# Kernel tuning notes

Hardware: AMD Instinct MI355X
Metric: run time of the kernel (lower is better)

Reference implementation:

```python
import jax, jax.numpy as jnp
import numpy as np

NUM_CHANNELS = 256
NUM_HEADS = 8
HEAD_DIM = NUM_CHANNELS // NUM_HEADS


def setup_inputs() -> dict:
    key = jax.random.key(0)
    k1, k2, k3, k4, k5 = jax.random.split(key, 5)
    C = NUM_CHANNELS
    s = 1.0 / np.sqrt(C)
    image = jax.random.normal(k1, (8, C, 32, 32), dtype=jnp.float32)
    # kqv_projection: Linear(C, 3C); mix_heads: Linear(C, C). Stored as [in, out].
    w_kqv = jax.random.uniform(k2, (C, 3 * C), minval=-s, maxval=s, dtype=jnp.float32)
    b_kqv = jax.random.uniform(k3, (3 * C,), minval=-s, maxval=s, dtype=jnp.float32)
    w_mix = jax.random.uniform(k4, (C, C), minval=-s, maxval=s, dtype=jnp.float32)
    b_mix = jax.random.uniform(k5, (C,), minval=-s, maxval=s, dtype=jnp.float32)
    return {"image": image, "w_kqv": w_kqv, "b_kqv": b_kqv, "w_mix": w_mix, "b_mix": b_mix}


def _masked_attention(seq, w_kqv, b_kqv, w_mix, b_mix):
    # seq: [N, T, C]
    N, T, C = seq.shape
    H, D = NUM_HEADS, HEAD_DIM
    projected = seq @ w_kqv + b_kqv            # [N, T, 3C]
    k, q, v = jnp.split(projected, 3, axis=-1)  # order: keys, queries, values
    # split heads -> [N, H, T, D]
    k = k.reshape(N, T, H, D).transpose(0, 2, 1, 3)
    q = q.reshape(N, T, H, D).transpose(0, 2, 1, 3)
    v = v.reshape(N, T, H, D).transpose(0, 2, 1, 3)
    logits = jnp.einsum('nhtd,nhsd->nhts', q, k) / jnp.sqrt(jnp.float32(D))
    causal = jnp.tril(jnp.ones((T, T), dtype=bool))
    logits = jnp.where(causal, logits, -jnp.inf)
    weights = jax.nn.softmax(logits, axis=-1)
    out = jnp.einsum('nhts,nhsd->nhtd', weights, v)  # [N, H, T, D]
    out = out.transpose(0, 2, 1, 3).reshape(N, T, C)  # combine heads
    return out @ w_mix + b_mix


def reference(image, w_kqv, b_kqv, w_mix, b_mix):
    N, C, Hh, Ww = image.shape
    seq = image.transpose(0, 2, 3, 1).reshape(N, Hh * Ww, C)
    attn = _masked_attention(seq, w_kqv, b_kqv, w_mix, b_mix)
    attn = attn.reshape(N, Hh, Ww, C).transpose(0, 3, 1, 2)
    return attn + image
```

## Files before the change

### kernel.cpp

```cpp
#include <hip/hip_runtime.h>
#include <math.h>

constexpr int NB  = 8;
constexpr int C   = 256;
constexpr int T   = 1024;
constexpr int NH  = 8;
constexpr int HD  = 32;
constexpr int C3  = 768;

constexpr float QSCALE = 0.25503489422229562f;

typedef __attribute__((ext_vector_type(8))) short bf16x8;
typedef __attribute__((ext_vector_type(4))) float f32x4;

__device__ inline short f2bf(float f) {
    unsigned u = __float_as_uint(f);
    u += 0x7FFF + ((u >> 16) & 1);
    return (short)(u >> 16);
}
__device__ inline short f2bf_trunc(float f) {
    return (short)(__float_as_uint(f) >> 16);
}

__global__ __launch_bounds__(256) void xpose_bf16(const float* __restrict__ image,
                                                  const float* __restrict__ wkqv,
                                                  const float* __restrict__ wmix,
                                                  short* __restrict__ seqb,
                                                  short* __restrict__ wkqvT,
                                                  short* __restrict__ wmixT) {
    __shared__ float Ld[32][33];
    const int bid = blockIdx.x;
    const float* src; short* dst; int srcStride;
    if (bid < 2048) {
        int nb = bid >> 8, rem = bid & 255, cb = rem >> 5, tb = rem & 31;
        src = image + ((size_t)nb * C + cb * 32) * T + tb * 32;
        dst = seqb + ((size_t)nb * T + tb * 32) * C + cb * 32;
        srcStride = T;
    } else if (bid < 2240) {
        int id = bid - 2048, jb = id >> 3, cb = id & 7;
        src = wkqv + (size_t)(cb * 32) * C3 + jb * 32;
        dst = wkqvT + (size_t)(jb * 32) * C + cb * 32;
        srcStride = C3;
    } else {
        int id = bid - 2240, jb = id >> 3, cb = id & 7;
        src = wmix + (size_t)(cb * 32) * C + jb * 32;
        dst = wmixT + (size_t)(jb * 32) * C + cb * 32;
        srcStride = C;
    }
    const int r = threadIdx.x >> 3, c4 = (threadIdx.x & 7) * 4;
    float4 v = *(const float4*)&src[(size_t)r * srcStride + c4];
    Ld[r][c4 + 0] = v.x; Ld[r][c4 + 1] = v.y; Ld[r][c4 + 2] = v.z; Ld[r][c4 + 3] = v.w;
    __syncthreads();
    short4 o = { f2bf(Ld[c4 + 0][r]), f2bf(Ld[c4 + 1][r]),
                 f2bf(Ld[c4 + 2][r]), f2bf(Ld[c4 + 3][r]) };
    *(short4*)&dst[(size_t)r * C + c4] = o;
}

__global__ __launch_bounds__(256) void kqv_mfma(const short* __restrict__ seqb,
                                                const short* __restrict__ wkqvT,
                                                const float* __restrict__ bkqv,
                                                short* __restrict__ Kb,
                                                short* __restrict__ Qb,
                                                short* __restrict__ Vb) {
    __shared__ __align__(16) short As[64][40];
    __shared__ __align__(16) short Bs[64][40];
    const int tid = threadIdx.x;
    const int n0 = blockIdx.x * 64;
    const int m0 = blockIdx.y * 64;
    const int nb = m0 >> 10, t0 = m0 & 1023;
    const int wv = tid >> 6, lane = tid & 63;
    const int m = lane & 15, quad = lane >> 4;
    const int sr = tid >> 2, sc8 = (tid & 3) * 8;

    f32x4 acc[4];
    const f32x4 z = {0.f, 0.f, 0.f, 0.f};
    #pragma unroll
    for (int j = 0; j < 4; ++j) acc[j] = z;

    bf16x8 areg = *(const bf16x8*)&seqb[(size_t)(m0 + sr) * C + sc8];
    bf16x8 breg = *(const bf16x8*)&wkqvT[(size_t)(n0 + sr) * C + sc8];

    for (int k0 = 0; k0 < C; k0 += 32) {
        __syncthreads();
        *(bf16x8*)&As[sr][sc8] = areg;
        *(bf16x8*)&Bs[sr][sc8] = breg;
        if (k0 + 32 < C) {
            areg = *(const bf16x8*)&seqb[(size_t)(m0 + sr) * C + k0 + 32 + sc8];
            breg = *(const bf16x8*)&wkqvT[(size_t)(n0 + sr) * C + k0 + 32 + sc8];
        }
        __syncthreads();
        bf16x8 a = *(const bf16x8*)&As[16 * wv + m][8 * quad];
        bf16x8 b[4];
        #pragma unroll
        for (int j = 0; j < 4; ++j) b[j] = *(const bf16x8*)&Bs[16 * j + m][8 * quad];
        #pragma unroll
        for (int j = 0; j < 4; ++j)
            acc[j] = __builtin_amdgcn_mfma_f32_16x16x32_bf16(a, b[j], acc[j], 0, 0, 0);
    }

    #pragma unroll
    for (int j = 0; j < 4; ++j) {
        int jj = n0 + 16 * j + m;
        int chunk = jj >> 8, hh = (jj >> 5) & 7, d = jj & 31;
        short* dst = (chunk == 0) ? Kb : (chunk == 1) ? Qb : Vb;
        float bias = bkqv[jj];
        float mul = (chunk == 1) ? QSCALE : 1.0f;
        size_t base = (size_t)(nb * NH + hh) * T * HD + d;
        int t = t0 + 16 * wv + 4 * quad;
        #pragma unroll
        for (int r = 0; r < 4; ++r)
            dst[base + (size_t)(t + r) * HD] = f2bf((acc[j][r] + bias) * mul);
    }
}

__global__ __launch_bounds__(256) void attn_mfma(const short* __restrict__ Kb,
                                                 const short* __restrict__ Qb,
                                                 const short* __restrict__ Vb,
                                                 short* __restrict__ attnb) {
    const int qb = 7 - blockIdx.x;
    const int h  = blockIdx.y;
    const int nb = blockIdx.z;
    const int tid  = threadIdx.x;
    const int wv   = tid >> 6;
    const int lane = tid & 63;
    const int m    = lane & 15;
    const int quad = lane >> 4;

    __shared__ __align__(16) short Qs[128][40];
    __shared__ __align__(16) short Ks[2][64][40];
    __shared__ __align__(16) short Vt[2][32][72];
    __shared__ __align__(16) short Ps[128][72];

    const int q0  = qb * 128;
    const int nst = 2 * qb + 2;
    const size_t hb = (size_t)(nb * NH + h) * T * HD;
    const short* Kp = Kb + hb;
    const short* Qp = Qb + hb;
    const short* Vp = Vb + hb;
    const int sr = tid >> 2, sc8 = (tid & 3) * 8;
    const f32x4 z = {0.f, 0.f, 0.f, 0.f};

    bf16x8 qr0  = *(const bf16x8*)&Qp[(size_t)(q0 + sr) * HD + sc8];
    bf16x8 qr1  = *(const bf16x8*)&Qp[(size_t)(q0 + 64 + sr) * HD + sc8];
    bf16x8 kreg = *(const bf16x8*)&Kp[(size_t)sr * HD + sc8];
    bf16x8 vreg = *(const bf16x8*)&Vp[(size_t)sr * HD + sc8];
    *(bf16x8*)&Qs[sr][sc8]      = qr0;
    *(bf16x8*)&Qs[64 + sr][sc8] = qr1;
    *(bf16x8*)&Ks[0][sr][sc8]   = kreg;
    #pragma unroll
    for (int i2 = 0; i2 < 8; ++i2) Vt[0][sc8 + i2][sr] = vreg[i2];

    f32x4 O[2][2] = {{z, z}, {z, z}};
    float lp[2][4] = {};

    for (int st = 0; st < nst; ++st) {
        const int p = st & 1;
        __syncthreads();
        if (st + 1 < nst) {
            kreg = *(const bf16x8*)&Kp[(size_t)((st + 1) * 64 + sr) * HD + sc8];
            vreg = *(const bf16x8*)&Vp[(size_t)((st + 1) * 64 + sr) * HD + sc8];
        }

        bf16x8 bk[4];
        #pragma unroll
        for (int j = 0; j < 4; ++j) bk[j] = *(const bf16x8*)&Ks[p][16 * j + m][8 * quad];
        f32x4 S[2][4];
        #pragma unroll
        for (int i = 0; i < 2; ++i) {
            bf16x8 aq = *(const bf16x8*)&Qs[32 * wv + 16 * i + m][8 * quad];
            #pragma unroll
            for (int j = 0; j < 4; ++j)
                S[i][j] = __builtin_amdgcn_mfma_f32_16x16x32_bf16(aq, bk[j], z, 0, 0, 0);
        }

        const bool msk = (st >= 2 * qb);
        const int s0 = st * 64;
        #pragma unroll
        for (int i = 0; i < 2; ++i) {
            const int qr_base = q0 + 32 * wv + 16 * i + 4 * quad;
            #pragma unroll
            for (int j = 0; j < 4; ++j) {
                const int sc = s0 + 16 * j + m;
                #pragma unroll
                for (int r = 0; r < 4; ++r) {
                    float e = __builtin_amdgcn_exp2f(S[i][j][r]);
                    if (msk && sc > qr_base + r) e = 0.f;
                    lp[i][r] += e;
                    Ps[32 * wv + 16 * i + 4 * quad + r][16 * j + m] = f2bf_trunc(e);
                }
            }
        }

        #pragma unroll
        for (int kc = 0; kc < 2; ++kc) {
            bf16x8 ap0 = *(const bf16x8*)&Ps[32 * wv + m][32 * kc + 8 * quad];
            bf16x8 ap1 = *(const bf16x8*)&Ps[32 * wv + 16 + m][32 * kc + 8 * quad];
            bf16x8 b0  = *(const bf16x8*)&Vt[p][m][32 * kc + 8 * quad];
            bf16x8 b1  = *(const bf16x8*)&Vt[p][16 + m][32 * kc + 8 * quad];
            O[0][0] = __builtin_amdgcn_mfma_f32_16x16x32_bf16(ap0, b0, O[0][0], 0, 0, 0);
            O[0][1] = __builtin_amdgcn_mfma_f32_16x16x32_bf16(ap0, b1, O[0][1], 0, 0, 0);
            O[1][0] = __builtin_amdgcn_mfma_f32_16x16x32_bf16(ap1, b0, O[1][0], 0, 0, 0);
            O[1][1] = __builtin_amdgcn_mfma_f32_16x16x32_bf16(ap1, b1, O[1][1], 0, 0, 0);
        }

        if (st + 1 < nst) {
            const int pn = p ^ 1;
            *(bf16x8*)&Ks[pn][sr][sc8] = kreg;
            #pragma unroll
            for (int i2 = 0; i2 < 8; ++i2) Vt[pn][sc8 + i2][sr] = vreg[i2];
        }
    }

    #pragma unroll
    for (int i = 0; i < 2; ++i)
        #pragma unroll
        for (int r = 0; r < 4; ++r) {
            float l = lp[i][r];
            l += __shfl_xor(l, 1);
            l += __shfl_xor(l, 2);
            l += __shfl_xor(l, 4);
            l += __shfl_xor(l, 8);
            float inv = 1.f / l;
            int row = q0 + 32 * wv + 16 * i + 4 * quad + r;
            short* op = attnb + ((size_t)(nb * T + row)) * C + h * HD;
            op[m]      = f2bf(O[i][0][r] * inv);
            op[16 + m] = f2bf(O[i][1][r] * inv);
        }
}

__global__ __launch_bounds__(256) void mix_mfma(const short* __restrict__ attnb,
                                                const short* __restrict__ wmixT,
                                                const float* __restrict__ bmix,
                                                const float* __restrict__ image,
                                                float* __restrict__ out) {
    __shared__ __align__(16) short As[64][40];
    __shared__ __align__(16) short Bs[64][40];
    const int tid = threadIdx.x;
    const int n0 = blockIdx.x * 64;
    const int m0 = blockIdx.y * 64;
    const int nb = m0 >> 10, t0 = m0 & 1023;
    const int wv = tid >> 6, lane = tid & 63;
    const int m = lane & 15, quad = lane >> 4;
    const int sr = tid >> 2, sc8 = (tid & 3) * 8;

    f32x4 acc[4];
    const f32x4 z = {0.f, 0.f, 0.f, 0.f};
    #pragma unroll
    for (int j = 0; j < 4; ++j) acc[j] = z;

    bf16x8 areg = *(const bf16x8*)&attnb[(size_t)(m0 + sr) * C + sc8];
    bf16x8 breg = *(const bf16x8*)&wmixT[(size_t)(n0 + sr) * C + sc8];

    for (int k0 = 0; k0 < C; k0 += 32) {
        __syncthreads();
        *(bf16x8*)&As[sr][sc8] = areg;
        *(bf16x8*)&Bs[sr][sc8] = breg;
        if (k0 + 32 < C) {
            areg = *(const bf16x8*)&attnb[(size_t)(m0 + sr) * C + k0 + 32 + sc8];
            breg = *(const bf16x8*)&wmixT[(size_t)(n0 + sr) * C + k0 + 32 + sc8];
        }
        __syncthreads();
        bf16x8 a = *(const bf16x8*)&As[16 * wv + m][8 * quad];
        bf16x8 b[4];
        #pragma unroll
        for (int j = 0; j < 4; ++j) b[j] = *(const bf16x8*)&Bs[16 * j + m][8 * quad];
        #pragma unroll
        for (int j = 0; j < 4; ++j)
            acc[j] = __builtin_amdgcn_mfma_f32_16x16x32_bf16(a, b[j], acc[j], 0, 0, 0);
    }

    const int tb = t0 + 16 * wv + 4 * quad;
    #pragma unroll
    for (int j = 0; j < 4; ++j) {
        int c = n0 + 16 * j + m;
        float bias = bmix[c];
        size_t o = (size_t)(nb * C + c) * T + tb;
        float4 img = *(const float4*)&image[o];
        float4 res = { acc[j][0] + bias + img.x,
                       acc[j][1] + bias + img.y,
                       acc[j][2] + bias + img.z,
                       acc[j][3] + bias + img.w };
        *(float4*)&out[o] = res;
    }
}

extern "C" void kernel_launch(void* const* d_in, const int* in_sizes, int n_in,
                              void* d_out, int out_size, void* d_ws, size_t ws_size,
                              hipStream_t stream) {
    const float* image = (const float*)d_in[0];
    const float* w_kqv = (const float*)d_in[1];
    const float* b_kqv = (const float*)d_in[2];
    const float* w_mix = (const float*)d_in[3];
    const float* b_mix = (const float*)d_in[4];
    float* out = (float*)d_out;

    short* seqb  = (short*)d_ws;
    short* wkqvT = seqb  + (size_t)NB * T * C;
    short* wmixT = wkqvT + (size_t)C3 * C;
    short* Kb    = wmixT + (size_t)C * C;
    short* Qb    = Kb    + (size_t)NB * NH * T * HD;
    short* Vb    = Qb    + (size_t)NB * NH * T * HD;
    short* attnb = Vb    + (size_t)NB * NH * T * HD;

    xpose_bf16<<<2304, 256, 0, stream>>>(image, w_kqv, w_mix, seqb, wkqvT, wmixT);
    kqv_mfma<<<dim3(C3 / 64, NB * T / 64), 256, 0, stream>>>(seqb, wkqvT, b_kqv, Kb, Qb, Vb);
    attn_mfma<<<dim3(8, NH, NB), 256, 0, stream>>>(Kb, Qb, Vb, attnb);
    mix_mfma<<<dim3(C / 64, NB * T / 64), 256, 0, stream>>>(attnb, wmixT, b_mix, image, out);
}
```

Baseline: 115.8 us.

## Fuse image transpose into KQV GEMM and pair causal query blocks in attention

The KQV projection now reads the fp32 NCHW image directly, converting to bf16 and transposing while staging its A tile into shared memory. This drops the separate image transpose pass and the seqb round-trip through global memory. The attention kernel now launches half as many blocks, and each block handles a short and a long causal query block (qb and 7-qb) so every block does the same amount of work. The cost is coalesced-but-strided fp32 loads in the GEMM and fewer, longer attention blocks, which lowers the available parallelism.

```diff
diff --git a/kernel.cpp b/kernel.cpp
--- a/kernel.cpp
+++ b/kernel.cpp
@@ -22,27 +22,20 @@
     return (short)(__float_as_uint(f) >> 16);
 }
 
-__global__ __launch_bounds__(256) void xpose_bf16(const float* __restrict__ image,
-                                                  const float* __restrict__ wkqv,
-                                                  const float* __restrict__ wmix,
-                                                  short* __restrict__ seqb,
-                                                  short* __restrict__ wkqvT,
-                                                  short* __restrict__ wmixT) {
+__global__ __launch_bounds__(256) void xpose_w(const float* __restrict__ wkqv,
+                                               const float* __restrict__ wmix,
+                                               short* __restrict__ wkqvT,
+                                               short* __restrict__ wmixT) {
     __shared__ float Ld[32][33];
     const int bid = blockIdx.x;
     const float* src; short* dst; int srcStride;
-    if (bid < 2048) {
-        int nb = bid >> 8, rem = bid & 255, cb = rem >> 5, tb = rem & 31;
-        src = image + ((size_t)nb * C + cb * 32) * T + tb * 32;
-        dst = seqb + ((size_t)nb * T + tb * 32) * C + cb * 32;
-        srcStride = T;
-    } else if (bid < 2240) {
-        int id = bid - 2048, jb = id >> 3, cb = id & 7;
+    if (bid < 192) {
+        int jb = bid >> 3, cb = bid & 7;
         src = wkqv + (size_t)(cb * 32) * C3 + jb * 32;
         dst = wkqvT + (size_t)(jb * 32) * C + cb * 32;
         srcStride = C3;
     } else {
-        int id = bid - 2240, jb = id >> 3, cb = id & 7;
+        int id = bid - 192, jb = id >> 3, cb = id & 7;
         src = wmix + (size_t)(cb * 32) * C + jb * 32;
         dst = wmixT + (size_t)(jb * 32) * C + cb * 32;
         srcStride = C;
@@ -56,7 +49,7 @@
     *(short4*)&dst[(size_t)r * C + c4] = o;
 }
 
-__global__ __launch_bounds__(256) void kqv_mfma(const short* __restrict__ seqb,
+__global__ __launch_bounds__(256) void kqv_mfma(const float* __restrict__ image,
                                                 const short* __restrict__ wkqvT,
                                                 const float* __restrict__ bkqv,
                                                 short* __restrict__ Kb,
@@ -71,21 +64,32 @@
     const int wv = tid >> 6, lane = tid & 63;
     const int m = lane & 15, quad = lane >> 4;
     const int sr = tid >> 2, sc8 = (tid & 3) * 8;
+    const int am = tid & 63, ak8 = (tid >> 6) * 8;
+
+    const float* imgn = image + (size_t)nb * C * T;
 
     f32x4 acc[4];
     const f32x4 z = {0.f, 0.f, 0.f, 0.f};
     #pragma unroll
     for (int j = 0; j < 4; ++j) acc[j] = z;
 
-    bf16x8 areg = *(const bf16x8*)&seqb[(size_t)(m0 + sr) * C + sc8];
+    float fa[8];
+    #pragma unroll
+    for (int i = 0; i < 8; ++i)
+        fa[i] = imgn[(size_t)(ak8 + i) * T + t0 + am];
     bf16x8 breg = *(const bf16x8*)&wkqvT[(size_t)(n0 + sr) * C + sc8];
 
     for (int k0 = 0; k0 < C; k0 += 32) {
         __syncthreads();
-        *(bf16x8*)&As[sr][sc8] = areg;
+        short4 alo = { f2bf(fa[0]), f2bf(fa[1]), f2bf(fa[2]), f2bf(fa[3]) };
+        short4 ahi = { f2bf(fa[4]), f2bf(fa[5]), f2bf(fa[6]), f2bf(fa[7]) };
+        *(short4*)&As[am][ak8]     = alo;
+        *(short4*)&As[am][ak8 + 4] = ahi;
         *(bf16x8*)&Bs[sr][sc8] = breg;
         if (k0 + 32 < C) {
-            areg = *(const bf16x8*)&seqb[(size_t)(m0 + sr) * C + k0 + 32 + sc8];
+            #pragma unroll
+            for (int i = 0; i < 8; ++i)
+                fa[i] = imgn[(size_t)(k0 + 32 + ak8 + i) * T + t0 + am];
             breg = *(const bf16x8*)&wkqvT[(size_t)(n0 + sr) * C + k0 + 32 + sc8];
         }
         __syncthreads();
@@ -117,7 +121,7 @@
                                                  const short* __restrict__ Qb,
                                                  const short* __restrict__ Vb,
                                                  short* __restrict__ attnb) {
-    const int qb = 7 - blockIdx.x;
+    const int qp = blockIdx.x;
     const int h  = blockIdx.y;
     const int nb = blockIdx.z;
     const int tid  = threadIdx.x;
@@ -131,8 +135,6 @@
     __shared__ __align__(16) short Vt[2][32][72];
     __shared__ __align__(16) short Ps[128][72];
 
-    const int q0  = qb * 128;
-    const int nst = 2 * qb + 2;
     const size_t hb = (size_t)(nb * NH + h) * T * HD;
     const short* Kp = Kb + hb;
     const short* Qp = Qb + hb;
@@ -140,92 +142,99 @@
     const int sr = tid >> 2, sc8 = (tid & 3) * 8;
     const f32x4 z = {0.f, 0.f, 0.f, 0.f};
 
-    bf16x8 qr0  = *(const bf16x8*)&Qp[(size_t)(q0 + sr) * HD + sc8];
-    bf16x8 qr1  = *(const bf16x8*)&Qp[(size_t)(q0 + 64 + sr) * HD + sc8];
-    bf16x8 kreg = *(const bf16x8*)&Kp[(size_t)sr * HD + sc8];
-    bf16x8 vreg = *(const bf16x8*)&Vp[(size_t)sr * HD + sc8];
-    *(bf16x8*)&Qs[sr][sc8]      = qr0;
-    *(bf16x8*)&Qs[64 + sr][sc8] = qr1;
-    *(bf16x8*)&Ks[0][sr][sc8]   = kreg;
-    #pragma unroll
-    for (int i2 = 0; i2 < 8; ++i2) Vt[0][sc8 + i2][sr] = vreg[i2];
-
-    f32x4 O[2][2] = {{z, z}, {z, z}};
-    float lp[2][4] = {};
-
-    for (int st = 0; st < nst; ++st) {
-        const int p = st & 1;
-        __syncthreads();
-        if (st + 1 < nst) {
-            kreg = *(const bf16x8*)&Kp[(size_t)((st + 1) * 64 + sr) * HD + sc8];
-            vreg = *(const bf16x8*)&Vp[(size_t)((st + 1) * 64 + sr) * HD + sc8];
+    #pragma unroll 1
+    for (int pp = 0; pp < 2; ++pp) {
+        const int qb  = pp ? 7 - qp : qp;
+        const int q0  = qb * 128;
+        const int nst = 2 * qb + 2;
+
+        __syncthreads();
+
+        *(bf16x8*)&Qs[sr][sc8]      = *(const bf16x8*)&Qp[(size_t)(q0 + sr) * HD + sc8];
+        *(bf16x8*)&Qs[64 + sr][sc8] = *(const bf16x8*)&Qp[(size_t)(q0 + 64 + sr) * HD + sc8];
+        bf16x8 kreg = *(const bf16x8*)&Kp[(size_t)sr * HD + sc8];
+        bf16x8 vreg = *(const bf16x8*)&Vp[(size_t)sr * HD + sc8];
+        *(bf16x8*)&Ks[0][sr][sc8] = kreg;
+        #pragma unroll
+        for (int i2 = 0; i2 < 8; ++i2) Vt[0][sc8 + i2][sr] = vreg[i2];
+
+        f32x4 O[2][2] = {{z, z}, {z, z}};
+        float lp[2][4] = {};
+
+        for (int st = 0; st < nst; ++st) {
+            const int p = st & 1;
+            __syncthreads();
+            if (st + 1 < nst) {
+                kreg = *(const bf16x8*)&Kp[(size_t)((st + 1) * 64 + sr) * HD + sc8];
+                vreg = *(const bf16x8*)&Vp[(size_t)((st + 1) * 64 + sr) * HD + sc8];
+            }
+
+            bf16x8 bk[4];
+            #pragma unroll
+            for (int j = 0; j < 4; ++j) bk[j] = *(const bf16x8*)&Ks[p][16 * j + m][8 * quad];
+            f32x4 S[2][4];
+            #pragma unroll
+            for (int i = 0; i < 2; ++i) {
+                bf16x8 aq = *(const bf16x8*)&Qs[32 * wv + 16 * i + m][8 * quad];
+                #pragma unroll
+                for (int j = 0; j < 4; ++j)
+                    S[i][j] = __builtin_amdgcn_mfma_f32_16x16x32_bf16(aq, bk[j], z, 0, 0, 0);
+            }
+
+            const bool msk = (st >= 2 * qb);
+            const int s0 = st * 64;
+            #pragma unroll
+            for (int i = 0; i < 2; ++i) {
+                const int qr_base = q0 + 32 * wv + 16 * i + 4 * quad;
+                #pragma unroll
+                for (int j = 0; j < 4; ++j) {
+                    const int sc = s0 + 16 * j + m;
+                    #pragma unroll
+                    for (int r = 0; r < 4; ++r) {
+                        float e = __builtin_amdgcn_exp2f(S[i][j][r]);
+                        if (msk && sc > qr_base + r) e = 0.f;
+                        lp[i][r] += e;
+                        Ps[32 * wv + 16 * i + 4 * quad + r][16 * j + m] = f2bf_trunc(e);
+                    }
+                }
+            }
+
+            #pragma unroll
+            for (int kc = 0; kc < 2; ++kc) {
+                bf16x8 ap0 = *(const bf16x8*)&Ps[32 * wv + m][32 * kc + 8 * quad];
+                bf16x8 ap1 = *(const bf16x8*)&Ps[32 * wv + 16 + m][32 * kc + 8 * quad];
+                bf16x8 b0  = *(const bf16x8*)&Vt[p][m][32 * kc + 8 * quad];
+                bf16x8 b1  = *(const bf16x8*)&Vt[p][16 + m][32 * kc + 8 * quad];
+                O[0][0] = __builtin_amdgcn_mfma_f32_16x16x32_bf16(ap0, b0, O[0][0], 0, 0, 0);
+                O[0][1] = __builtin_amdgcn_mfma_f32_16x16x32_bf16(ap0, b1, O[0][1], 0, 0, 0);
+                O[1][0] = __builtin_amdgcn_mfma_f32_16x16x32_bf16(ap1, b0, O[1][0], 0, 0, 0);
+                O[1][1] = __builtin_amdgcn_mfma_f32_16x16x32_bf16(ap1, b1, O[1][1], 0, 0, 0);
+            }
+
+            if (st + 1 < nst) {
+                const int pn = p ^ 1;
+                *(bf16x8*)&Ks[pn][sr][sc8] = kreg;
+                #pragma unroll
+                for (int i2 = 0; i2 < 8; ++i2) Vt[pn][sc8 + i2][sr] = vreg[i2];
+            }
         }
 
-        bf16x8 bk[4];
-        #pragma unroll
-        for (int j = 0; j < 4; ++j) bk[j] = *(const bf16x8*)&Ks[p][16 * j + m][8 * quad];
-        f32x4 S[2][4];
-        #pragma unroll
-        for (int i = 0; i < 2; ++i) {
-            bf16x8 aq = *(const bf16x8*)&Qs[32 * wv + 16 * i + m][8 * quad];
-            #pragma unroll
-            for (int j = 0; j < 4; ++j)
-                S[i][j] = __builtin_amdgcn_mfma_f32_16x16x32_bf16(aq, bk[j], z, 0, 0, 0);
-        }
-
-        const bool msk = (st >= 2 * qb);
-        const int s0 = st * 64;
-        #pragma unroll
-        for (int i = 0; i < 2; ++i) {
-            const int qr_base = q0 + 32 * wv + 16 * i + 4 * quad;
-            #pragma unroll
-            for (int j = 0; j < 4; ++j) {
-                const int sc = s0 + 16 * j + m;
-                #pragma unroll
-                for (int r = 0; r < 4; ++r) {
-                    float e = __builtin_amdgcn_exp2f(S[i][j][r]);
-                    if (msk && sc > qr_base + r) e = 0.f;
-                    lp[i][r] += e;
-                    Ps[32 * wv + 16 * i + 4 * quad + r][16 * j + m] = f2bf_trunc(e);
-                }
-            }
-        }
-
-        #pragma unroll
-        for (int kc = 0; kc < 2; ++kc) {
-            bf16x8 ap0 = *(const bf16x8*)&Ps[32 * wv + m][32 * kc + 8 * quad];
-            bf16x8 ap1 = *(const bf16x8*)&Ps[32 * wv + 16 + m][32 * kc + 8 * quad];
-            bf16x8 b0  = *(const bf16x8*)&Vt[p][m][32 * kc + 8 * quad];
-            bf16x8 b1  = *(const bf16x8*)&Vt[p][16 + m][32 * kc + 8 * quad];
-            O[0][0] = __builtin_amdgcn_mfma_f32_16x16x32_bf16(ap0, b0, O[0][0], 0, 0, 0);
-            O[0][1] = __builtin_amdgcn_mfma_f32_16x16x32_bf16(ap0, b1, O[0][1], 0, 0, 0);
-            O[1][0] = __builtin_amdgcn_mfma_f32_16x16x32_bf16(ap1, b0, O[1][0], 0, 0, 0);
-            O[1][1] = __builtin_amdgcn_mfma_f32_16x16x32_bf16(ap1, b1, O[1][1], 0, 0, 0);
-        }
-
-        if (st + 1 < nst) {
-            const int pn = p ^ 1;
-            *(bf16x8*)&Ks[pn][sr][sc8] = kreg;
-            #pragma unroll
-            for (int i2 = 0; i2 < 8; ++i2) Vt[pn][sc8 + i2][sr] = vreg[i2];
-        }
-    }
-
-    #pragma unroll
-    for (int i = 0; i < 2; ++i)
-        #pragma unroll
-        for (int r = 0; r < 4; ++r) {
-            float l = lp[i][r];
-            l += __shfl_xor(l, 1);
-            l += __shfl_xor(l, 2);
-            l += __shfl_xor(l, 4);
-            l += __shfl_xor(l, 8);
-            float inv = 1.f / l;
-            int row = q0 + 32 * wv + 16 * i + 4 * quad + r;
-            short* op = attnb + ((size_t)(nb * T + row)) * C + h * HD;
-            op[m]      = f2bf(O[i][0][r] * inv);
-            op[16 + m] = f2bf(O[i][1][r] * inv);
-        }
+        #pragma unroll
+        for (int i = 0; i < 2; ++i)
+            #pragma unroll
+            for (int r = 0; r < 4; ++r) {
+                float l = lp[i][r];
+                l += __shfl_xor(l, 1);
+                l += __shfl_xor(l, 2);
+                l += __shfl_xor(l, 4);
+                l += __shfl_xor(l, 8);
+                float inv = 1.f / l;
+                int row = q0 + 32 * wv + 16 * i + 4 * quad + r;
+                short* op = attnb + ((size_t)(nb * T + row)) * C + h * HD;
+                op[m]      = f2bf(O[i][0][r] * inv);
+                op[16 + m] = f2bf(O[i][1][r] * inv);
+            }
+    }
 }
 
 __global__ __launch_bounds__(256) void mix_mfma(const short* __restrict__ attnb,
@@ -294,16 +303,15 @@
     const float* b_mix = (const float*)d_in[4];
     float* out = (float*)d_out;
 
-    short* seqb  = (short*)d_ws;
-    short* wkqvT = seqb  + (size_t)NB * T * C;
+    short* wkqvT = (short*)d_ws;
     short* wmixT = wkqvT + (size_t)C3 * C;
     short* Kb    = wmixT + (size_t)C * C;
     short* Qb    = Kb    + (size_t)NB * NH * T * HD;
     short* Vb    = Qb    + (size_t)NB * NH * T * HD;
     short* attnb = Vb    + (size_t)NB * NH * T * HD;
 
-    xpose_bf16<<<2304, 256, 0, stream>>>(image, w_kqv, w_mix, seqb, wkqvT, wmixT);
-    kqv_mfma<<<dim3(C3 / 64, NB * T / 64), 256, 0, stream>>>(seqb, wkqvT, b_kqv, Kb, Qb, Vb);
-    attn_mfma<<<dim3(8, NH, NB), 256, 0, stream>>>(Kb, Qb, Vb, attnb);
+    xpose_w<<<256, 256, 0, stream>>>(w_kqv, w_mix, wkqvT, wmixT);
+    kqv_mfma<<<dim3(C3 / 64, NB * T / 64), 256, 0, stream>>>(image, wkqvT, b_kqv, Kb, Qb, Vb);
+    attn_mfma<<<dim3(4, NH, NB), 256, 0, stream>>>(Kb, Qb, Vb, attnb);
     mix_mfma<<<dim3(C / 64, NB * T / 64), 256, 0, stream>>>(attnb, wmixT, b_mix, image, out);
 }
```

After: 112.7 us. 2.7% less time.
